# Performance work log

Hardware: AMD Instinct MI355X
Metric: run time of the kernel (lower is better)

The kernel has to match this reference:

```python
import jax, jax.numpy as jnp
import numpy as np

N_NODES = 100000
N_EDGES = 1600000
D = 128
HID = 256  # min(2*D, 256)
D_OUT = 128
BN_EPS = 1e-5


def setup_inputs() -> dict:
    key = jax.random.key(0)
    ks = jax.random.split(key, 16)
    s = 0.05
    inp = {
        "x": jax.random.normal(ks[0], (N_NODES, D), dtype=jnp.float32),
        "edges": jax.random.randint(ks[1], (2, N_EDGES), 0, N_NODES, dtype=jnp.int32),
        # affine_before_rnn: Linear(D, D)
        "W_aff": jax.random.normal(ks[2], (D, D), dtype=jnp.float32) * s,
        "b_aff": jnp.zeros((D,), dtype=jnp.float32),
        # GRUCell(D, D)
        "W_ih": jax.random.normal(ks[3], (3 * D, D), dtype=jnp.float32) * s,
        "b_ih": jnp.zeros((3 * D,), dtype=jnp.float32),
        "W_hh": jax.random.normal(ks[4], (3 * D, D), dtype=jnp.float32) * s,
        "b_hh": jnp.zeros((3 * D,), dtype=jnp.float32),
        # merge_layer: Linear(2*D, D)
        "W_merge": jax.random.normal(ks[5], (D, 2 * D), dtype=jnp.float32) * s,
        "b_merge": jnp.zeros((D,), dtype=jnp.float32),
        # learnable self-connection weight
        "eps": jnp.asarray(1.0, dtype=jnp.float32),
        # backbone: Linear(D, HID) -> relu -> Linear(HID, D_OUT) -> relu -> BatchNorm1d
        "W1": jax.random.normal(ks[6], (HID, D), dtype=jnp.float32) * s,
        "b1": jnp.zeros((HID,), dtype=jnp.float32),
        "W2": jax.random.normal(ks[7], (D_OUT, HID), dtype=jnp.float32) * s,
        "b2": jnp.zeros((D_OUT,), dtype=jnp.float32),
        "gamma": jnp.ones((D_OUT,), dtype=jnp.float32),
        "beta": jnp.zeros((D_OUT,), dtype=jnp.float32),
    }
    return inp


def reference(x, edges, W_aff, b_aff, W_ih, b_ih, W_hh, b_hh,
              W_merge, b_merge, eps, W1, b1, W2, b2, gamma, beta):
    src, dst = edges[0], edges[1]
    n = x.shape[0]

    # ---- aggregation 1: 'sum' -> scatter-sum of neighbor features ----
    agg_sum = jax.ops.segment_sum(x[src], dst, num_segments=n)  # (N, D)

    # ---- aggregation 2: 'rnn-max' -> affine, scatter-max, GRUCell ----
    xi = x @ W_aff.T + b_aff
    agg_max = jax.ops.segment_max(xi[src], dst, num_segments=n)  # (N, D)
    agg_max = jnp.where(jnp.isfinite(agg_max), agg_max, 0.0)  # empty segments -> 0

    # GRUCell: input = aggregated neighbors, hidden = original node features
    gi = agg_max @ W_ih.T + b_ih  # (N, 3D)
    gh = x @ W_hh.T + b_hh        # (N, 3D)
    ir, iz, inn = jnp.split(gi, 3, axis=1)
    hr, hz, hn = jnp.split(gh, 3, axis=1)
    r = jax.nn.sigmoid(ir + hr)
    z = jax.nn.sigmoid(iz + hz)
    ncand = jnp.tanh(inn + r * hn)
    rnn_out = (1.0 - z) * ncand + z * x  # (N, D)

    # ---- merge ('cat') ----
    h = jnp.concatenate([agg_sum, rnn_out], axis=1) @ W_merge.T + b_merge  # (N, D)

    # ---- learnable self-connection ----
    h = h + eps * x

    # ---- backbone: dense -> relu -> dense -> relu -> batchnorm1d (train mode) ----
    h = jax.nn.relu(h @ W1.T + b1)
    h = jax.nn.relu(h @ W2.T + b2)
    mean = jnp.mean(h, axis=0)
    var = jnp.mean(jnp.square(h - mean), axis=0)  # biased batch variance
    out = gamma * (h - mean) * jax.lax.rsqrt(var + BN_EPS) + beta
    return out
```

## Files before the change

kernel.cpp:

```cpp
#include <hip/hip_runtime.h>
#include <hip/hip_bf16.h>
#include <math.h>

using bf16 = __hip_bfloat16;
typedef __attribute__((ext_vector_type(8))) short bf16x8;
typedef __attribute__((ext_vector_type(4))) float f32x4;

__device__ __forceinline__ float b2f(unsigned short u) {
  return __uint_as_float(((unsigned)u) << 16);
}
__device__ __forceinline__ unsigned short f2b(float f) {
  bf16 h = __float2bfloat16(f);
  return *reinterpret_cast<unsigned short*>(&h);
}
__device__ __forceinline__ ushort4 f2b4(float4 v) {
  return make_ushort4(f2b(v.x), f2b(v.y), f2b(v.z), f2b(v.w));
}

__global__ __launch_bounds__(256) void mgemm_k(
    const unsigned short* __restrict__ A, int lda, const float* __restrict__ W,
    const float* __restrict__ bias, unsigned short* __restrict__ Cb, int ldc,
    int N, int M, int K) {
  constexpr int LDA = 72;
  __shared__ unsigned short As[128 * LDA];
  __shared__ unsigned short Ws[128 * LDA];

  const int tid = threadIdx.x;
  const int lane = tid & 63;
  const int wave = tid >> 6;
  const int row0 = blockIdx.y * 128;
  const int m0 = blockIdx.x * 128;
  const int rowhalf = (wave & 1) * 64;
  const int colhalf = (wave >> 1) * 64;
  const int l15 = lane & 15;
  const int quad = lane >> 4;

  f32x4 acc[4][4] = {};

  for (int kc = 0; kc < K; kc += 64) {
#pragma unroll
    for (int i = 0; i < 4; i++) {
      int idx = tid + i * 256;
      int r = idx >> 3;
      int k8 = (idx & 7) * 8;
      int row = row0 + r;
      ushort4 u0 = make_ushort4(0, 0, 0, 0), u1 = u0;
      if (row < N) {
        const unsigned short* s = A + (size_t)row * lda + kc + k8;
        u0 = *(const ushort4*)s;
        u1 = *(const ushort4*)(s + 4);
      }
      *(ushort4*)&As[r * LDA + k8] = u0;
      *(ushort4*)&As[r * LDA + k8 + 4] = u1;
    }
#pragma unroll
    for (int i = 0; i < 8; i++) {
      int idx = tid + i * 256;
      int r = idx >> 4;
      int k4 = idx & 15;
      float4 v = *(const float4*)(W + (size_t)(m0 + r) * K + kc + k4 * 4);
      *(ushort4*)&Ws[r * LDA + k4 * 4] = f2b4(v);
    }
    __syncthreads();
#pragma unroll
    for (int ks = 0; ks < 2; ks++) {
      const int ko = ks * 32 + quad * 8;
      bf16x8 af[4], wf[4];
#pragma unroll
      for (int ri = 0; ri < 4; ri++)
        af[ri] = *(const bf16x8*)&As[(rowhalf + ri * 16 + l15) * LDA + ko];
#pragma unroll
      for (int ci = 0; ci < 4; ci++)
        wf[ci] = *(const bf16x8*)&Ws[(colhalf + ci * 16 + l15) * LDA + ko];
#pragma unroll
      for (int ri = 0; ri < 4; ri++)
#pragma unroll
        for (int ci = 0; ci < 4; ci++)
          acc[ri][ci] = __builtin_amdgcn_mfma_f32_16x16x32_bf16(
              af[ri], wf[ci], acc[ri][ci], 0, 0, 0);
    }
    __syncthreads();
  }
#pragma unroll
  for (int ci = 0; ci < 4; ci++) {
    const int col = m0 + colhalf + ci * 16 + l15;
    const float bv = bias[col];
#pragma unroll
    for (int ri = 0; ri < 4; ri++) {
      const int rbase = row0 + rowhalf + ri * 16 + quad * 4;
#pragma unroll
      for (int r = 0; r < 4; r++) {
        int row = rbase + r;
        if (row >= N) continue;
        Cb[(size_t)row * ldc + col] = f2b(acc[ri][ci][r] + bv);
      }
    }
  }
}

__global__ __launch_bounds__(512, 4) void grubb_k(
    const unsigned short* __restrict__ aggm,
    const unsigned short* __restrict__ xcat,
    const unsigned short* __restrict__ aggs,
    const unsigned short* __restrict__ Wbig,
    const float* __restrict__ bias_big,
    const unsigned short* __restrict__ Wmb, const float* __restrict__ bm,
    const unsigned short* __restrict__ W1b, const float* __restrict__ b1,
    const unsigned short* __restrict__ W2b, const float* __restrict__ b2,
    const float* __restrict__ epsp, float* __restrict__ out,
    float* __restrict__ pstats, int N) {
  constexpr int LDA = 264;
  constexpr int LDH = 136;
  __shared__ unsigned short As[64 * LDA];
  __shared__ unsigned short Acat[64 * LDA];
  __shared__ float sbn[128], qbn[128];
  unsigned short* Hd = As;
  unsigned short* Hp = Acat;

  const int tid = threadIdx.x;
  const int lane = tid & 63;
  const int wave = tid >> 6;
  const int l15 = lane & 15;
  const int quad = lane >> 4;
  const int row0 = blockIdx.x * 64;
  if (tid < 128) {
    sbn[tid] = 0.f;
    qbn[tid] = 0.f;
  }
  const float ep = epsp[0];
  const int f = wave * 16 + l15;

  {
    int r = tid >> 3;
    int q = tid & 7;
    int row = row0 + r;
    int k32 = q * 32;
    uint4 u[4] = {};
    uint4 v[2] = {};
    if (row < N) {
      const unsigned short* s = (k32 < 128)
                                    ? aggm + (size_t)row * 128 + k32
                                    : xcat + (size_t)row * 256 + (k32 - 128);
#pragma unroll
      for (int i = 0; i < 4; i++) u[i] = *(const uint4*)(s + i * 8);
      const unsigned short* s2 = aggs + (size_t)row * 128 + q * 16;
      v[0] = *(const uint4*)s2;
      v[1] = *(const uint4*)(s2 + 8);
    }
#pragma unroll
    for (int i = 0; i < 4; i++) *(uint4*)&As[r * LDA + k32 + i * 8] = u[i];
    *(uint4*)&Acat[r * LDA + q * 16] = v[0];
    *(uint4*)&Acat[r * LDA + q * 16 + 8] = v[1];
  }
  __syncthreads();

  {
    const unsigned short* wp[4];
#pragma unroll
    for (int g = 0; g < 4; g++)
      wp[g] = Wbig +
              (size_t)((wave >> 1) * 128 + (g + 4 * (wave & 1)) * 16 + l15) *
                  256 +
              quad * 8;
    f32x4 acc[4][4] = {};
#pragma unroll
    for (int ks = 0; ks < 8; ks++) {
      const int ko = ks * 32 + quad * 8;
      bf16x8 af[4];
#pragma unroll
      for (int ri = 0; ri < 4; ri++)
        af[ri] = *(const bf16x8*)&As[(ri * 16 + l15) * LDA + ko];
#pragma unroll
      for (int g = 0; g < 4; g++) {
        if (g == 2 && ks >= 4) continue;
        if (g == 3 && ks < 4) continue;
        bf16x8 wf = *(const bf16x8*)(wp[g] + ks * 32);
#pragma unroll
        for (int ri = 0; ri < 4; ri++)
          acc[ri][g] = __builtin_amdgcn_mfma_f32_16x16x32_bf16(
              af[ri], wf, acc[ri][g], 0, 0, 0);
      }
    }
    const float br = bias_big[f];
    const float bz = bias_big[128 + f];
    const float bi = bias_big[256 + f];
    const float bh = bias_big[384 + f];
#pragma unroll
    for (int ri = 0; ri < 4; ri++) {
#pragma unroll
      for (int r = 0; r < 4; r++) {
        int rl = ri * 16 + quad * 4 + r;
        float rg = 1.f / (1.f + __expf(-(acc[ri][0][r] + br)));
        float zg = 1.f / (1.f + __expf(-(acc[ri][1][r] + bz)));
        float a = acc[ri][2][r] + bi + rg * (acc[ri][3][r] + bh);
        float t = 1.f - 2.f / (__expf(2.f * fabsf(a)) + 1.f);
        float nc = copysignf(t, a);
        float xv = b2f(As[rl * LDA + 128 + f]);
        Acat[rl * LDA + 128 + f] = f2b((1.f - zg) * nc + zg * xv);
      }
    }
  }
  __syncthreads();

  f32x4 accm[4] = {};
  {
    const unsigned short* wptr = Wmb + (size_t)f * 256 + quad * 8;
#pragma unroll
    for (int ks = 0; ks < 8; ks++) {
      const int ko = ks * 32 + quad * 8;
      bf16x8 w0 = *(const bf16x8*)(wptr + ks * 32);
#pragma unroll
      for (int ri = 0; ri < 4; ri++) {
        bf16x8 af = *(const bf16x8*)&Acat[(ri * 16 + l15) * LDA + ko];
        accm[ri] = __builtin_amdgcn_mfma_f32_16x16x32_bf16(af, w0, accm[ri],
                                                           0, 0, 0);
      }
    }
  }
  __syncthreads();
  {
    float bv = bm[f];
#pragma unroll
    for (int ri = 0; ri < 4; ri++) {
#pragma unroll
      for (int r = 0; r < 4; r++) {
        int rl = ri * 16 + quad * 4 + r;
        float v = accm[ri][r] + bv + ep * b2f(As[rl * LDA + 128 + f]);
        Hp[rl * LDH + f] = f2b(v);
      }
    }
  }
  __syncthreads();

  f32x4 acc3[4] = {};
#pragma unroll
  for (int hh = 0; hh < 2; hh++) {
    f32x4 acc2[4] = {};
    {
      const unsigned short* wptr =
          W1b + (size_t)(hh * 128 + f) * 128 + quad * 8;
#pragma unroll
      for (int ks = 0; ks < 4; ks++) {
        const int ko = ks * 32 + quad * 8;
        bf16x8 w0 = *(const bf16x8*)(wptr + ks * 32);
#pragma unroll
        for (int ri = 0; ri < 4; ri++) {
          bf16x8 af = *(const bf16x8*)&Hp[(ri * 16 + l15) * LDH + ko];
          acc2[ri] = __builtin_amdgcn_mfma_f32_16x16x32_bf16(af, w0, acc2[ri],
                                                             0, 0, 0);
        }
      }
    }
    __syncthreads();
    {
      float bv = b1[hh * 128 + f];
#pragma unroll
      for (int ri = 0; ri < 4; ri++) {
#pragma unroll
        for (int r = 0; r < 4; r++) {
          int rl = ri * 16 + quad * 4 + r;
          Hd[rl * LDH + f] = f2b(fmaxf(acc2[ri][r] + bv, 0.f));
        }
      }
    }
    __syncthreads();
    {
      const unsigned short* wptr =
          W2b + (size_t)f * 256 + hh * 128 + quad * 8;
#pragma unroll
      for (int ks = 0; ks < 4; ks++) {
        const int ko = ks * 32 + quad * 8;
        bf16x8 w0 = *(const bf16x8*)(wptr + ks * 32);
#pragma unroll
        for (int ri = 0; ri < 4; ri++) {
          bf16x8 af = *(const bf16x8*)&Hd[(ri * 16 + l15) * LDH + ko];
          acc3[ri] = __builtin_amdgcn_mfma_f32_16x16x32_bf16(af, w0, acc3[ri],
                                                             0, 0, 0);
        }
      }
    }
  }
  {
    float bv = b2[f];
    float s = 0.f, q = 0.f;
#pragma unroll
    for (int ri = 0; ri < 4; ri++) {
#pragma unroll
      for (int r = 0; r < 4; r++) {
        int rl = ri * 16 + quad * 4 + r;
        int row = row0 + rl;
        if (row >= N) continue;
        float v = fmaxf(acc3[ri][r] + bv, 0.f);
        out[(size_t)row * 128 + f] = v;
        s += v;
        q += v * v;
      }
    }
    atomicAdd(&sbn[f], s);
    atomicAdd(&qbn[f], q);
  }
  __syncthreads();
  if (tid < 128) {
    float* p = pstats + (size_t)blockIdx.x * 256;
    p[tid] = sbn[tid];
    p[128 + tid] = qbn[tid];
  }
}

__global__ __launch_bounds__(256) void bnred_k(const float* __restrict__ pstats,
                                               float* __restrict__ stats,
                                               int nb) {
  int t = threadIdx.x;
  float s = 0.f;
  for (int b = blockIdx.x; b < nb; b += gridDim.x)
    s += pstats[(size_t)b * 256 + t];
  atomicAdd(&stats[t], s);
}

__global__ __launch_bounds__(256) void prep_k(
    const float* __restrict__ W_ih, const float* __restrict__ b_ih,
    const float* __restrict__ W_hh, const float* __restrict__ b_hh,
    const float* __restrict__ Wm, const float* __restrict__ W1,
    const float* __restrict__ W2, unsigned short* __restrict__ Wbig,
    unsigned short* __restrict__ Wmb, unsigned short* __restrict__ W1b,
    unsigned short* __restrict__ W2b, float* __restrict__ bias_big,
    float* __restrict__ stats, int* __restrict__ deg, int N) {
  int idx = blockIdx.x * 256 + threadIdx.x;
  if (idx < N) deg[idx] = 0;
  if (idx < 32768) {
    int mp = idx >> 6;
    int k4 = (idx & 63) * 4;
    int w = mp >> 7, ci = (mp >> 4) & 7, l15 = mp & 15;
    int g = ci & 3, fi = ci >> 2;
    int f = w * 32 + fi * 16 + l15;
    const float* src = nullptr;
    int koff = 0;
    if (g <= 1) {
      int m = g * 128 + f;
      if (k4 < 128) { src = W_ih + (size_t)m * 128; koff = k4; }
      else          { src = W_hh + (size_t)m * 128; koff = k4 - 128; }
    } else if (g == 2) {
      if (k4 < 128) { src = W_ih + (size_t)(256 + f) * 128; koff = k4; }
    } else {
      if (k4 >= 128) { src = W_hh + (size_t)(256 + f) * 128; koff = k4 - 128; }
    }
    ushort4 o = make_ushort4(0, 0, 0, 0);
    if (src) o = f2b4(*(const float4*)(src + koff));
    *(ushort4*)&Wbig[(size_t)mp * 256 + k4] = o;
  }
  if (idx < 8192) {
    int m = idx >> 6;
    int k4 = (idx & 63) * 4;
    *(ushort4*)&Wmb[(size_t)m * 256 + k4] =
        f2b4(*(const float4*)(Wm + (size_t)m * 256 + k4));
    *(ushort4*)&W2b[(size_t)m * 256 + k4] =
        f2b4(*(const float4*)(W2 + (size_t)m * 256 + k4));
    int m2 = idx >> 5;
    int k42 = (idx & 31) * 4;
    *(ushort4*)&W1b[(size_t)m2 * 128 + k42] =
        f2b4(*(const float4*)(W1 + (size_t)m2 * 128 + k42));
  }
  if (blockIdx.x == 0) {
    int t = threadIdx.x;
    stats[t] = 0.f;
#pragma unroll
    for (int h = 0; h < 2; h++) {
      int mm = t + h * 256;
      float b;
      if (mm < 256) b = b_ih[mm] + b_hh[mm];
      else if (mm < 384) b = b_ih[mm];
      else b = b_hh[mm - 128];
      bias_big[mm] = b;
    }
  }
}

__global__ __launch_bounds__(256) void cvthist_k(
    const int* __restrict__ edges, int* __restrict__ deg, int E,
    const float* __restrict__ x, unsigned short* __restrict__ xcat,
    int ngroups, int eblk) {
  if ((int)blockIdx.x < eblk) {
    int e = blockIdx.x * 256 + threadIdx.x;
    if (e < E) atomicAdd(&deg[edges[(size_t)E + e]], 1);
  } else {
    int g = (blockIdx.x - eblk) * 256 + threadIdx.x;
    if (g >= ngroups) return;
    int n = g >> 5;
    int j = (g & 31) * 4;
    float4 v = *(const float4*)&x[(size_t)n * 128 + j];
    *(ushort4*)&xcat[(size_t)n * 256 + j] = f2b4(v);
  }
}

__global__ __launch_bounds__(256) void scan1_k(const int* __restrict__ deg,
                                               int* __restrict__ off,
                                               int* __restrict__ bsums, int N) {
  __shared__ int s[256];
  int t = threadIdx.x;
  int i = blockIdx.x * 256 + t;
  int v = (i < N) ? deg[i] : 0;
  s[t] = v;
  __syncthreads();
#pragma unroll
  for (int d = 1; d < 256; d <<= 1) {
    int u = (t >= d) ? s[t - d] : 0;
    __syncthreads();
    s[t] += u;
    __syncthreads();
  }
  if (i < N) off[i] = s[t] - v;
  if (t == 255) bsums[blockIdx.x] = s[255];
}

__global__ __launch_bounds__(512) void scan2_k(int* __restrict__ bsums,
                                               int nb) {
  __shared__ int s[512];
  int t = threadIdx.x;
  int v = (t < nb) ? bsums[t] : 0;
  s[t] = v;
  __syncthreads();
#pragma unroll
  for (int d = 1; d < 512; d <<= 1) {
    int u = (t >= d) ? s[t - d] : 0;
    __syncthreads();
    s[t] += u;
    __syncthreads();
  }
  if (t < nb) bsums[t] = s[t] - v;
}

__global__ __launch_bounds__(256) void scan3_k(int* __restrict__ off,
                                               const int* __restrict__ bsums,
                                               int* __restrict__ binoff,
                                               int* __restrict__ bincur,
                                               int N, int E, int NB) {
  int i = blockIdx.x * 256 + threadIdx.x;
  if (i < N) {
    int o = off[i] + bsums[blockIdx.x];
    off[i] = o;
    if ((i & 511) == 0) {
      binoff[i >> 9] = o;
      bincur[i >> 9] = o;
    }
  }
  if (i == 0) {
    off[N] = E;
    binoff[NB] = E;
  }
}

__global__ __launch_bounds__(256) void edgepart_k(const int* __restrict__ edges,
                                                  int* __restrict__ bincur,
                                                  int* __restrict__ part,
                                                  int E, int NB) {
  __shared__ int cnt[256];
  const int tid = threadIdx.x;
  if (tid < NB) cnt[tid] = 0;
  __syncthreads();
  int sv[16], dv[16];
  const int e0 = blockIdx.x * 4096;
#pragma unroll
  for (int i = 0; i < 16; i++) {
    int e = e0 + i * 256 + tid;
    int s = 0, d = -1;
    if (e < E) {
      s = edges[e];
      d = edges[(size_t)E + e];
    }
    sv[i] = s;
    dv[i] = d;
    if (d >= 0) atomicAdd(&cnt[d >> 9], 1);
  }
  __syncthreads();
  if (tid < NB) {
    int c = cnt[tid];
    int base = c ? atomicAdd(&bincur[tid], c) : 0;
    cnt[tid] = base;
  }
  __syncthreads();
#pragma unroll
  for (int i = 0; i < 16; i++) {
    int d = dv[i];
    if (d < 0) continue;
    int p = atomicAdd(&cnt[d >> 9], 1);
    part[p] = (sv[i] << 9) | (d & 511);
  }
}

__global__ __launch_bounds__(1024) void fill2_k(const int* __restrict__ off,
                                                const int* __restrict__ binoff,
                                                const int* __restrict__ part,
                                                int* __restrict__ bucket,
                                                int N) {
  __shared__ int scur[512];
  const int b = blockIdx.x;
  const int n0 = b << 9;
  const int tid = threadIdx.x;
  if (tid < 512) {
    int node = n0 + tid;
    scur[tid] = (node < N) ? off[node] : 0;
  }
  __syncthreads();
  const int j0 = binoff[b];
  const int j1 = binoff[b + 1];
  for (int j = j0 + tid; j < j1; j += 1024) {
    int p = part[j];
    int pos = atomicAdd(&scur[p & 511], 1);
    bucket[pos] = p >> 9;
  }
}

__global__ __launch_bounds__(256) void gather_k(
    const int* __restrict__ off, const int* __restrict__ bucket,
    const unsigned short* __restrict__ xcat, unsigned short* __restrict__ aggm,
    unsigned short* __restrict__ aggs, int N) {
  int node = blockIdx.x * 4 + (threadIdx.x >> 6);
  if (node >= N) return;
  const int lane = threadIdx.x & 63;
  const int half = lane >> 5;
  const int f = (lane & 31) * 4;
  const int j0 = off[node], jend = off[node + 1];
  float s0 = 0.f, s1 = 0.f, s2 = 0.f, s3 = 0.f;
  float m0 = -INFINITY, m1 = -INFINITY, m2 = -INFINITY, m3 = -INFINITY;
  int jj = j0 + half;
  int p0 = (jj < jend) ? bucket[jj] : 0;
  int p1 = (jj + 2 < jend) ? bucket[jj + 2] : 0;
  for (; jj < jend; jj += 2) {
    int src = p0;
    p0 = p1;
    p1 = (jj + 4 < jend) ? bucket[jj + 4] : 0;
    ushort4 a = *(const ushort4*)(xcat + (size_t)src * 256 + f);
    ushort4 b = *(const ushort4*)(xcat + (size_t)src * 256 + 128 + f);
    s0 += b2f(a.x);
    s1 += b2f(a.y);
    s2 += b2f(a.z);
    s3 += b2f(a.w);
    m0 = fmaxf(m0, b2f(b.x));
    m1 = fmaxf(m1, b2f(b.y));
    m2 = fmaxf(m2, b2f(b.z));
    m3 = fmaxf(m3, b2f(b.w));
  }
  s0 += __shfl_xor(s0, 32);
  s1 += __shfl_xor(s1, 32);
  s2 += __shfl_xor(s2, 32);
  s3 += __shfl_xor(s3, 32);
  m0 = fmaxf(m0, __shfl_xor(m0, 32));
  m1 = fmaxf(m1, __shfl_xor(m1, 32));
  m2 = fmaxf(m2, __shfl_xor(m2, 32));
  m3 = fmaxf(m3, __shfl_xor(m3, 32));
  if (half == 0) {
    bool nz = jend > j0;
    ushort4 mv = nz ? make_ushort4(f2b(m0), f2b(m1), f2b(m2), f2b(m3))
                    : make_ushort4(0, 0, 0, 0);
    *(ushort4*)&aggm[(size_t)node * 128 + f] = mv;
    *(ushort4*)&aggs[(size_t)node * 128 + f] =
        make_ushort4(f2b(s0), f2b(s1), f2b(s2), f2b(s3));
  }
}

__global__ __launch_bounds__(256) void bn_apply_k(
    float* __restrict__ out, const float* __restrict__ stats,
    const float* __restrict__ gamma, const float* __restrict__ beta,
    float invn, int nd4) {
  int g = blockIdx.x * 256 + threadIdx.x;
  if (g >= nd4) return;
  int d = (g & 31) * 4;
  float4 v = ((float4*)out)[g];
  float o[4] = {v.x, v.y, v.z, v.w};
#pragma unroll
  for (int i = 0; i < 4; i++) {
    float mean = stats[d + i] * invn;
    float var = fmaxf(stats[128 + d + i] * invn - mean * mean, 0.f);
    float sc = gamma[d + i] * rsqrtf(var + 1e-5f);
    o[i] = (o[i] - mean) * sc + beta[d + i];
  }
  ((float4*)out)[g] = make_float4(o[0], o[1], o[2], o[3]);
}

extern "C" void kernel_launch(void* const* d_in, const int* in_sizes, int n_in,
                              void* d_out, int out_size, void* d_ws,
                              size_t ws_size, hipStream_t stream) {
  (void)n_in;
  (void)out_size;
  (void)ws_size;
  const float* x = (const float*)d_in[0];
  const int* edges = (const int*)d_in[1];
  const float* W_aff = (const float*)d_in[2];
  const float* b_aff = (const float*)d_in[3];
  const float* W_ih = (const float*)d_in[4];
  const float* b_ih = (const float*)d_in[5];
  const float* W_hh = (const float*)d_in[6];
  const float* b_hh = (const float*)d_in[7];
  const float* W_merge = (const float*)d_in[8];
  const float* b_merge = (const float*)d_in[9];
  const float* epsp = (const float*)d_in[10];
  const float* W1 = (const float*)d_in[11];
  const float* b1 = (const float*)d_in[12];
  const float* W2 = (const float*)d_in[13];
  const float* b2 = (const float*)d_in[14];
  const float* gamma = (const float*)d_in[15];
  const float* beta = (const float*)d_in[16];

  const int N = in_sizes[0] / 128;
  const int E = in_sizes[1] / 2;
  const size_t nd = (size_t)N * 128;
  const int NB = (N + 511) >> 9;
  const int gblk = (N + 63) / 64;

  char* base = (char*)d_ws;
  unsigned short* xcat = (unsigned short*)base;
  unsigned short* aggs = (unsigned short*)(base + (size_t)N * 512);
  unsigned short* aggm = (unsigned short*)(base + (size_t)N * 1024);
  unsigned short* Wbig = (unsigned short*)(base + (size_t)N * 1280);
  unsigned short* Wmb = Wbig + 512 * 256;
  unsigned short* W1b = Wmb + 128 * 256;
  unsigned short* W2b = W1b + 256 * 128;
  float* bias_big = (float*)(W2b + 128 * 256);
  float* stats = bias_big + 512;
  int* deg = (int*)(stats + 512);
  int* off = deg + N;
  int* binoff = off + N + 1;
  int* bincur = binoff + NB + 1;
  int* bucket = bincur + NB;
  int* bsums = bucket + E;
  float* pstats = (float*)(bsums + ((N + 255) / 256));
  float* out = (float*)d_out;
  int* part = (int*)d_out;

  const int ny = (N + 127) / 128;
  const int nblk = (N + 255) / 256;
  const int eblk = (E + 255) / 256;
  const int cvtblk = (int)((nd / 4 + 255) / 256);
  const int pgrid = nblk > 128 ? nblk : 128;
  dim3 blk(256);

  prep_k<<<pgrid, blk, 0, stream>>>(W_ih, b_ih, W_hh, b_hh, W_merge, W1, W2,
                                    Wbig, Wmb, W1b, W2b, bias_big, stats, deg,
                                    N);
  cvthist_k<<<eblk + cvtblk, blk, 0, stream>>>(edges, deg, E, x, xcat,
                                               (int)(nd / 4), eblk);
  scan1_k<<<nblk, blk, 0, stream>>>(deg, off, bsums, N);
  scan2_k<<<1, 512, 0, stream>>>(bsums, nblk);
  scan3_k<<<nblk, blk, 0, stream>>>(off, bsums, binoff, bincur, N, E, NB);
  edgepart_k<<<(E + 4095) / 4096, blk, 0, stream>>>(edges, bincur, part, E, NB);
  fill2_k<<<NB, dim3(1024), 0, stream>>>(off, binoff, part, bucket, N);

  mgemm_k<<<dim3(1, ny), blk, 0, stream>>>(xcat, 256, W_aff, b_aff, xcat + 128,
                                           256, N, 128, 128);
  gather_k<<<(N + 3) / 4, blk, 0, stream>>>(off, bucket, xcat, aggm, aggs, N);
  grubb_k<<<gblk, dim3(512), 0, stream>>>(aggm, xcat, aggs, Wbig, bias_big,
                                          Wmb, b_merge, W1b, b1, W2b, b2,
                                          epsp, out, pstats, N);
  bnred_k<<<64, blk, 0, stream>>>(pstats, stats, gblk);
  bn_apply_k<<<(int)((nd / 4 + 255) / 256), blk, 0, stream>>>(
      out, stats, gamma, beta, 1.f / (float)N, (int)(nd / 4));
}
```

Baseline: 560.7 us.

## Fuse x bf16 conversion into affine GEMM, store pre-BN output as bf16, set MFMA priority

The fp32-to-bf16 conversion of x is folded into the affine GEMM kernel, which now reads fp32 x, writes the bf16 copy into xcat and computes the affine half in one pass. This removes a separate read and write pass over x. The backbone kernel now writes its pre-BatchNorm activations as bf16 into a reused workspace buffer instead of fp32 into the output, which halves that round trip before bn_apply. s_setprio is raised around the MFMA loops. The bf16 intermediate adds rounding error before normalization, and the histogram kernel loses its overlap with the conversion work.

```diff
diff --git a/kernel.cpp b/kernel.cpp
--- a/kernel.cpp
+++ b/kernel.cpp
@@ -18,9 +18,8 @@
 }
 
 __global__ __launch_bounds__(256) void mgemm_k(
-    const unsigned short* __restrict__ A, int lda, const float* __restrict__ W,
-    const float* __restrict__ bias, unsigned short* __restrict__ Cb, int ldc,
-    int N, int M, int K) {
+    const float* __restrict__ x, unsigned short* __restrict__ xcat,
+    const float* __restrict__ W, const float* __restrict__ bias, int N) {
   constexpr int LDA = 72;
   __shared__ unsigned short As[128 * LDA];
   __shared__ unsigned short Ws[128 * LDA];
@@ -28,8 +27,7 @@
   const int tid = threadIdx.x;
   const int lane = tid & 63;
   const int wave = tid >> 6;
-  const int row0 = blockIdx.y * 128;
-  const int m0 = blockIdx.x * 128;
+  const int row0 = blockIdx.x * 128;
   const int rowhalf = (wave & 1) * 64;
   const int colhalf = (wave >> 1) * 64;
   const int l15 = lane & 15;
@@ -37,7 +35,7 @@
 
   f32x4 acc[4][4] = {};
 
-  for (int kc = 0; kc < K; kc += 64) {
+  for (int kc = 0; kc < 128; kc += 64) {
 #pragma unroll
     for (int i = 0; i < 4; i++) {
       int idx = tid + i * 256;
@@ -46,9 +44,11 @@
       int row = row0 + r;
       ushort4 u0 = make_ushort4(0, 0, 0, 0), u1 = u0;
       if (row < N) {
-        const unsigned short* s = A + (size_t)row * lda + kc + k8;
-        u0 = *(const ushort4*)s;
-        u1 = *(const ushort4*)(s + 4);
+        const float* s = x + (size_t)row * 128 + kc + k8;
+        u0 = f2b4(*(const float4*)s);
+        u1 = f2b4(*(const float4*)(s + 4));
+        *(ushort4*)&xcat[(size_t)row * 256 + kc + k8] = u0;
+        *(ushort4*)&xcat[(size_t)row * 256 + kc + k8 + 4] = u1;
       }
       *(ushort4*)&As[r * LDA + k8] = u0;
       *(ushort4*)&As[r * LDA + k8 + 4] = u1;
@@ -58,7 +58,7 @@
       int idx = tid + i * 256;
       int r = idx >> 4;
       int k4 = idx & 15;
-      float4 v = *(const float4*)(W + (size_t)(m0 + r) * K + kc + k4 * 4);
+      float4 v = *(const float4*)(W + (size_t)r * 128 + kc + k4 * 4);
       *(ushort4*)&Ws[r * LDA + k4 * 4] = f2b4(v);
     }
     __syncthreads();
@@ -83,7 +83,7 @@
   }
 #pragma unroll
   for (int ci = 0; ci < 4; ci++) {
-    const int col = m0 + colhalf + ci * 16 + l15;
+    const int col = colhalf + ci * 16 + l15;
     const float bv = bias[col];
 #pragma unroll
     for (int ri = 0; ri < 4; ri++) {
@@ -92,7 +92,7 @@
       for (int r = 0; r < 4; r++) {
         int row = rbase + r;
         if (row >= N) continue;
-        Cb[(size_t)row * ldc + col] = f2b(acc[ri][ci][r] + bv);
+        xcat[(size_t)row * 256 + 128 + col] = f2b(acc[ri][ci][r] + bv);
       }
     }
   }
@@ -107,7 +107,7 @@
     const unsigned short* __restrict__ Wmb, const float* __restrict__ bm,
     const unsigned short* __restrict__ W1b, const float* __restrict__ b1,
     const unsigned short* __restrict__ W2b, const float* __restrict__ b2,
-    const float* __restrict__ epsp, float* __restrict__ out,
+    const float* __restrict__ epsp, unsigned short* __restrict__ hout,
     float* __restrict__ pstats, int N) {
   constexpr int LDA = 264;
   constexpr int LDH = 136;
@@ -163,6 +163,7 @@
                   256 +
               quad * 8;
     f32x4 acc[4][4] = {};
+    __builtin_amdgcn_s_setprio(1);
 #pragma unroll
     for (int ks = 0; ks < 8; ks++) {
       const int ko = ks * 32 + quad * 8;
@@ -181,6 +182,7 @@
               af[ri], wf, acc[ri][g], 0, 0, 0);
       }
     }
+    __builtin_amdgcn_s_setprio(0);
     const float br = bias_big[f];
     const float bz = bias_big[128 + f];
     const float bi = bias_big[256 + f];
@@ -205,6 +207,7 @@
   f32x4 accm[4] = {};
   {
     const unsigned short* wptr = Wmb + (size_t)f * 256 + quad * 8;
+    __builtin_amdgcn_s_setprio(1);
 #pragma unroll
     for (int ks = 0; ks < 8; ks++) {
       const int ko = ks * 32 + quad * 8;
@@ -216,6 +219,7 @@
                                                            0, 0, 0);
       }
     }
+    __builtin_amdgcn_s_setprio(0);
   }
   __syncthreads();
   {
@@ -239,6 +243,7 @@
     {
       const unsigned short* wptr =
           W1b + (size_t)(hh * 128 + f) * 128 + quad * 8;
+      __builtin_amdgcn_s_setprio(1);
 #pragma unroll
       for (int ks = 0; ks < 4; ks++) {
         const int ko = ks * 32 + quad * 8;
@@ -250,6 +255,7 @@
                                                              0, 0, 0);
         }
       }
+      __builtin_amdgcn_s_setprio(0);
     }
     __syncthreads();
     {
@@ -267,6 +273,7 @@
     {
       const unsigned short* wptr =
           W2b + (size_t)f * 256 + hh * 128 + quad * 8;
+      __builtin_amdgcn_s_setprio(1);
 #pragma unroll
       for (int ks = 0; ks < 4; ks++) {
         const int ko = ks * 32 + quad * 8;
@@ -278,6 +285,7 @@
                                                              0, 0, 0);
         }
       }
+      __builtin_amdgcn_s_setprio(0);
     }
   }
   {
@@ -291,7 +299,7 @@
         int row = row0 + rl;
         if (row >= N) continue;
         float v = fmaxf(acc3[ri][r] + bv, 0.f);
-        out[(size_t)row * 128 + f] = v;
+        hout[(size_t)row * 128 + f] = f2b(v);
         s += v;
         q += v * v;
       }
@@ -375,21 +383,10 @@
   }
 }
 
-__global__ __launch_bounds__(256) void cvthist_k(
-    const int* __restrict__ edges, int* __restrict__ deg, int E,
-    const float* __restrict__ x, unsigned short* __restrict__ xcat,
-    int ngroups, int eblk) {
-  if ((int)blockIdx.x < eblk) {
-    int e = blockIdx.x * 256 + threadIdx.x;
-    if (e < E) atomicAdd(&deg[edges[(size_t)E + e]], 1);
-  } else {
-    int g = (blockIdx.x - eblk) * 256 + threadIdx.x;
-    if (g >= ngroups) return;
-    int n = g >> 5;
-    int j = (g & 31) * 4;
-    float4 v = *(const float4*)&x[(size_t)n * 128 + j];
-    *(ushort4*)&xcat[(size_t)n * 256 + j] = f2b4(v);
-  }
+__global__ __launch_bounds__(256) void hist_k(const int* __restrict__ edges,
+                                              int* __restrict__ deg, int E) {
+  int e = blockIdx.x * 256 + threadIdx.x;
+  if (e < E) atomicAdd(&deg[edges[(size_t)E + e]], 1);
 }
 
 __global__ __launch_bounds__(256) void scan1_k(const int* __restrict__ deg,
@@ -559,14 +556,14 @@
 }
 
 __global__ __launch_bounds__(256) void bn_apply_k(
-    float* __restrict__ out, const float* __restrict__ stats,
-    const float* __restrict__ gamma, const float* __restrict__ beta,
-    float invn, int nd4) {
+    float* __restrict__ out, const unsigned short* __restrict__ hout,
+    const float* __restrict__ stats, const float* __restrict__ gamma,
+    const float* __restrict__ beta, float invn, int nd4) {
   int g = blockIdx.x * 256 + threadIdx.x;
   if (g >= nd4) return;
   int d = (g & 31) * 4;
-  float4 v = ((float4*)out)[g];
-  float o[4] = {v.x, v.y, v.z, v.w};
+  ushort4 hv = ((const ushort4*)hout)[g];
+  float o[4] = {b2f(hv.x), b2f(hv.y), b2f(hv.z), b2f(hv.w)};
 #pragma unroll
   for (int i = 0; i < 4; i++) {
     float mean = stats[d + i] * invn;
@@ -625,33 +622,31 @@
   int* bsums = bucket + E;
   float* pstats = (float*)(bsums + ((N + 255) / 256));
   float* out = (float*)d_out;
+  unsigned short* hout = aggs;
   int* part = (int*)d_out;
 
   const int ny = (N + 127) / 128;
   const int nblk = (N + 255) / 256;
   const int eblk = (E + 255) / 256;
-  const int cvtblk = (int)((nd / 4 + 255) / 256);
   const int pgrid = nblk > 128 ? nblk : 128;
   dim3 blk(256);
 
   prep_k<<<pgrid, blk, 0, stream>>>(W_ih, b_ih, W_hh, b_hh, W_merge, W1, W2,
                                     Wbig, Wmb, W1b, W2b, bias_big, stats, deg,
                                     N);
-  cvthist_k<<<eblk + cvtblk, blk, 0, stream>>>(edges, deg, E, x, xcat,
-                                               (int)(nd / 4), eblk);
+  hist_k<<<eblk, blk, 0, stream>>>(edges, deg, E);
   scan1_k<<<nblk, blk, 0, stream>>>(deg, off, bsums, N);
   scan2_k<<<1, 512, 0, stream>>>(bsums, nblk);
   scan3_k<<<nblk, blk, 0, stream>>>(off, bsums, binoff, bincur, N, E, NB);
   edgepart_k<<<(E + 4095) / 4096, blk, 0, stream>>>(edges, bincur, part, E, NB);
   fill2_k<<<NB, dim3(1024), 0, stream>>>(off, binoff, part, bucket, N);
 
-  mgemm_k<<<dim3(1, ny), blk, 0, stream>>>(xcat, 256, W_aff, b_aff, xcat + 128,
-                                           256, N, 128, 128);
+  mgemm_k<<<ny, blk, 0, stream>>>(x, xcat, W_aff, b_aff, N);
   gather_k<<<(N + 3) / 4, blk, 0, stream>>>(off, bucket, xcat, aggm, aggs, N);
   grubb_k<<<gblk, dim3(512), 0, stream>>>(aggm, xcat, aggs, Wbig, bias_big,
                                           Wmb, b_merge, W1b, b1, W2b, b2,
-                                          epsp, out, pstats, N);
+                                          epsp, hout, pstats, N);
   bnred_k<<<64, blk, 0, stream>>>(pstats, stats, gblk);
   bn_apply_k<<<(int)((nd / 4 + 255) / 256), blk, 0, stream>>>(
-      out, stats, gamma, beta, 1.f / (float)N, (int)(nd / 4));
-}
+      out, hout, stats, gamma, beta, 1.f / (float)N, (int)(nd / 4));
+}
```

Result: faster. 547.6 us, median of 2 (-2.3%).
